# Optimization experiments

Hardware: AMD Instinct MI355X
Metric: run time of the kernel (lower is better)

Reference implementation:

```python
import jax, jax.numpy as jnp
import numpy as np

def setup_inputs() -> dict:
    key = jax.random.key(0)
    k1, k2 = jax.random.split(key)
    user_embeddings = jax.random.normal(k1, (1024, 64), dtype=jnp.float32)
    movie_embeddings = jax.random.normal(k2, (50000, 64), dtype=jnp.float32)
    return {"user_embeddings": user_embeddings, "movie_embeddings": movie_embeddings}

def reference(user_embeddings, movie_embeddings):
    # square_of_sum[b,m] = (sum_k u[b,k] m[m,k])^2
    square_of_sum = jnp.matmul(user_embeddings, movie_embeddings.T) ** 2
    # sum_of_square[b,m] = sum_k (u[b,k] m[m,k])^2 = (u^2) @ (m^2)^T
    # Algebraically identical to the original's broadcast (B, M, D) intermediate,
    # but computed as a second GEMM on squared embeddings.
    sum_of_square = jnp.matmul(user_embeddings ** 2, (movie_embeddings ** 2).T)
    interaction = 0.5 * (square_of_sum - sum_of_square)
    return interaction
```

## Files before the change

### kernel.cpp

```cpp
#include <hip/hip_runtime.h>

typedef short short8 __attribute__((ext_vector_type(8)));
typedef float f32x4 __attribute__((ext_vector_type(4)));

#define DK 64

__device__ __forceinline__ short f2bf(float x) {
    unsigned u = __builtin_bit_cast(unsigned, x);
    unsigned r = (u + 0x7fffu + ((u >> 16) & 1u)) >> 16;
    return (short)r;
}

__device__ __forceinline__ void gl_lds16(const void* g, void* l) {
    __builtin_amdgcn_global_load_lds(
        (const __attribute__((address_space(1))) unsigned int*)g,
        (__attribute__((address_space(3))) unsigned int*)l, 16, 0, 0);
}

__global__ __launch_bounds__(256)
void fm_convert(const float* __restrict__ U, const float* __restrict__ M,
                short* __restrict__ ws, int NU, int NM, int NUP, int NMP) {
    int id = blockIdx.x * blockDim.x + threadIdx.x;
    int total = (NUP + NMP) * 8;
    if (id >= total) return;
    int rowg = id >> 3;
    int p = id & 7;
    const float* src; short *dv, *dq; int row, nvalid;
    if (rowg < NUP) {
        row = rowg; src = U; dv = ws; dq = ws + (size_t)NUP * DK; nvalid = NU;
    } else {
        row = rowg - NUP; src = M;
        dv = ws + (size_t)2 * NUP * DK; dq = dv + (size_t)NMP * DK; nvalid = NM;
    }
    short8 v8 = {0,0,0,0,0,0,0,0}, q8 = {0,0,0,0,0,0,0,0};
    if (row < nvalid) {
        int cp = p ^ (row & 7);
        const float* s = src + (size_t)row * DK + cp * 8;
        float4 a = *(const float4*)(s);
        float4 b = *(const float4*)(s + 4);
        v8 = (short8){ f2bf(a.x), f2bf(a.y), f2bf(a.z), f2bf(a.w),
                       f2bf(b.x), f2bf(b.y), f2bf(b.z), f2bf(b.w) };
        q8 = (short8){ f2bf(a.x*a.x), f2bf(a.y*a.y), f2bf(a.z*a.z), f2bf(a.w*a.w),
                       f2bf(b.x*b.x), f2bf(b.y*b.y), f2bf(b.z*b.z), f2bf(b.w*b.w) };
    }
    *(short8*)(dv + (size_t)row * DK + p * 8) = v8;
    *(short8*)(dq + (size_t)row * DK + p * 8) = q8;
}

#define BM 64
#define BN 128

__global__ __launch_bounds__(256, 3)
void fm_gemm(const short* __restrict__ ws, float* __restrict__ out,
             int NM, int NMP, int NUP) {
    __shared__ short sA [BM * DK];
    __shared__ short sA2[BM * DK];
    __shared__ short sB [BN * DK];
    __shared__ short sB2[BN * DK];

    const int t = threadIdx.x;
    const int lane = t & 63;
    const int w = t >> 6;
    const int wr = w >> 1;
    const int wc = w & 1;
    const int lr = lane & 15;
    const int lk = lane >> 4;

    const int mbase = blockIdx.x * BM;
    const int nbase = blockIdx.y * BN;

    const short* gU  = ws;
    const short* gU2 = ws + (size_t)NUP * DK;
    const short* gM  = ws + (size_t)2 * NUP * DK;
    const short* gM2 = gM + (size_t)NMP * DK;

    {
        const short* srcA  = gU  + (size_t)mbase * DK;
        const short* srcA2 = gU2 + (size_t)mbase * DK;
        const short* srcB  = gM  + (size_t)nbase * DK;
        const short* srcB2 = gM2 + (size_t)nbase * DK;
        const int lo = lane * 8;
#pragma unroll
        for (int i = 0; i < 2; ++i) {
            const int ch = w * 2 + i;
            gl_lds16(srcA  + ch * 512 + lo, sA  + ch * 512);
            gl_lds16(srcA2 + ch * 512 + lo, sA2 + ch * 512);
        }
#pragma unroll
        for (int i = 0; i < 4; ++i) {
            const int ch = w * 4 + i;
            gl_lds16(srcB  + ch * 512 + lo, sB  + ch * 512);
            gl_lds16(srcB2 + ch * 512 + lo, sB2 + ch * 512);
        }
    }
    __syncthreads();

    f32x4 accS[2][4], accQ[2][4];
#pragma unroll
    for (int m = 0; m < 2; ++m)
#pragma unroll
        for (int n = 0; n < 4; ++n) {
            accS[m][n] = (f32x4){0.f, 0.f, 0.f, 0.f};
            accQ[m][n] = (f32x4){0.f, 0.f, 0.f, 0.f};
        }

#pragma unroll
    for (int ks = 0; ks < 2; ++ks) {
        const int c = ks * 4 + lk;
        short8 af[2], a2f[2], bf[4], b2f[4];
#pragma unroll
        for (int m = 0; m < 2; ++m) {
            const int row = wr * 32 + m * 16 + lr;
            const int idx = row * DK + ((c ^ (row & 7)) << 3);
            af[m]  = *(const short8*)&sA [idx];
            a2f[m] = *(const short8*)&sA2[idx];
        }
#pragma unroll
        for (int n = 0; n < 4; ++n) {
            const int row = wc * 64 + n * 16 + lr;
            const int idx = row * DK + ((c ^ (row & 7)) << 3);
            bf[n]  = *(const short8*)&sB [idx];
            b2f[n] = *(const short8*)&sB2[idx];
        }
#pragma unroll
        for (int m = 0; m < 2; ++m)
#pragma unroll
            for (int n = 0; n < 4; ++n) {
                accS[m][n] = __builtin_amdgcn_mfma_f32_16x16x32_bf16(af[m],  bf[n],  accS[m][n], 0, 0, 0);
                accQ[m][n] = __builtin_amdgcn_mfma_f32_16x16x32_bf16(a2f[m], b2f[n], accQ[m][n], 0, 0, 0);
            }
    }

#pragma unroll
    for (int m = 0; m < 2; ++m) {
        const int grow0 = mbase + wr * 32 + m * 16 + lk * 4;
#pragma unroll
        for (int n = 0; n < 4; ++n) {
            const int gcol = nbase + wc * 64 + n * 16 + lr;
            if (gcol < NM) {
                f32x4 s = accS[m][n];
                f32x4 q = accQ[m][n];
#pragma unroll
                for (int r = 0; r < 4; ++r)
                    out[(size_t)(grow0 + r) * NM + gcol] = 0.5f * (s[r] * s[r] - q[r]);
            }
        }
    }
}

__global__ __launch_bounds__(256, 2)
void fm_fallback(const float* __restrict__ U, const float* __restrict__ M,
                 float* __restrict__ out, int NU, int NM) {
    __shared__ short sA [128 * DK];
    __shared__ short sA2[128 * DK];
    __shared__ short sB [128 * DK];
    __shared__ short sB2[128 * DK];

    const int t = threadIdx.x;
    const int lane = t & 63;
    const int w = t >> 6;
    const int wr = w >> 1;
    const int wc = w & 1;
    const int lr = lane & 15;
    const int lk = lane >> 4;

    const int mbase = blockIdx.x * 128;
    const int nbase = blockIdx.y * 128;

    const int r0 = t >> 4;
    const int c4 = t & 15;
    const int chunk = c4 >> 1;
    const int sub = c4 & 1;

    typedef short short4v __attribute__((ext_vector_type(4)));
#pragma unroll
    for (int i = 0; i < 8; ++i) {
        const int r = r0 + i * 16;
        const int sidx = r * DK + ((chunk ^ (r & 7)) << 3) + (sub << 2);
        {
            float4 v = make_float4(0.f, 0.f, 0.f, 0.f);
            const int gr = mbase + r;
            if (gr < NU) v = *(const float4*)(U + (size_t)gr * DK + c4 * 4);
            short4v b  = { f2bf(v.x), f2bf(v.y), f2bf(v.z), f2bf(v.w) };
            short4v b2 = { f2bf(v.x*v.x), f2bf(v.y*v.y), f2bf(v.z*v.z), f2bf(v.w*v.w) };
            *(short4v*)&sA[sidx] = b; *(short4v*)&sA2[sidx] = b2;
        }
        {
            float4 v = make_float4(0.f, 0.f, 0.f, 0.f);
            const int gr = nbase + r;
            if (gr < NM) v = *(const float4*)(M + (size_t)gr * DK + c4 * 4);
            short4v b  = { f2bf(v.x), f2bf(v.y), f2bf(v.z), f2bf(v.w) };
            short4v b2 = { f2bf(v.x*v.x), f2bf(v.y*v.y), f2bf(v.z*v.z), f2bf(v.w*v.w) };
            *(short4v*)&sB[sidx] = b; *(short4v*)&sB2[sidx] = b2;
        }
    }
    __syncthreads();

    f32x4 accS[4][4], accQ[4][4];
#pragma unroll
    for (int m = 0; m < 4; ++m)
#pragma unroll
        for (int n = 0; n < 4; ++n) {
            accS[m][n] = (f32x4){0.f,0.f,0.f,0.f};
            accQ[m][n] = (f32x4){0.f,0.f,0.f,0.f};
        }
#pragma unroll
    for (int ks = 0; ks < 2; ++ks) {
        short8 af[4], a2f[4], bfr[4], b2f[4];
        const int c = ks * 4 + lk;
#pragma unroll
        for (int m = 0; m < 4; ++m) {
            const int row = wr * 64 + m * 16 + lr;
            const int idx = row * DK + ((c ^ (row & 7)) << 3);
            af[m] = *(const short8*)&sA[idx]; a2f[m] = *(const short8*)&sA2[idx];
        }
#pragma unroll
        for (int n = 0; n < 4; ++n) {
            const int row = wc * 64 + n * 16 + lr;
            const int idx = row * DK + ((c ^ (row & 7)) << 3);
            bfr[n] = *(const short8*)&sB[idx]; b2f[n] = *(const short8*)&sB2[idx];
        }
#pragma unroll
        for (int m = 0; m < 4; ++m)
#pragma unroll
            for (int n = 0; n < 4; ++n) {
                accS[m][n] = __builtin_amdgcn_mfma_f32_16x16x32_bf16(af[m],  bfr[n], accS[m][n], 0, 0, 0);
                accQ[m][n] = __builtin_amdgcn_mfma_f32_16x16x32_bf16(a2f[m], b2f[n], accQ[m][n], 0, 0, 0);
            }
    }
#pragma unroll
    for (int m = 0; m < 4; ++m) {
        const int grow0 = mbase + wr * 64 + m * 16 + lk * 4;
#pragma unroll
        for (int n = 0; n < 4; ++n) {
            const int gcol = nbase + wc * 64 + n * 16 + lr;
            if (gcol < NM) {
                f32x4 s = accS[m][n]; f32x4 q = accQ[m][n];
#pragma unroll
                for (int r = 0; r < 4; ++r) {
                    const int grow = grow0 + r;
                    if (grow < NU)
                        out[(size_t)grow * NM + gcol] = 0.5f * (s[r]*s[r] - q[r]);
                }
            }
        }
    }
}

extern "C" void kernel_launch(void* const* d_in, const int* in_sizes, int n_in,
                              void* d_out, int out_size, void* d_ws, size_t ws_size,
                              hipStream_t stream) {
    const float* U = (const float*)d_in[0];
    const float* M = (const float*)d_in[1];
    float* out = (float*)d_out;
    const int NU = in_sizes[0] / DK;
    const int NM = in_sizes[1] / DK;
    const int NUP = ((NU + 63) / 64) * 64;
    const int NMP = ((NM + 127) / 128) * 128;
    const size_t need = (size_t)(NUP + NMP) * DK * 2 * sizeof(short);

    if ((NU % 64 == 0) && ws_size >= need) {
        short* ws = (short*)d_ws;
        const int tasks = (NUP + NMP) * 8;
        fm_convert<<<(tasks + 255) / 256, 256, 0, stream>>>(U, M, ws, NU, NM, NUP, NMP);
        dim3 grid(NU / BM, NMP / BN);
        fm_gemm<<<grid, dim3(256), 0, stream>>>(ws, out, NM, NMP, NUP);
    } else {
        dim3 grid((NU + 127) / 128, (NM + 127) / 128);
        fm_fallback<<<grid, dim3(256), 0, stream>>>(U, M, out, NU, NM);
    }
}
```

Before: 59.96 us.

## Drop LDS staging, keep movie fragments in registers and loop over user tiles

The GEMM kernel no longer stages tiles in shared memory. Each wave loads its 32 movie rows' bf16 fragments straight into registers once and reuses them across four 64-row user tiles, loading user fragments directly from global memory, which the L2 cache should serve because the user matrix is small. Operands are swapped so each lane holds four consecutive output columns, which allows 16-byte nontemporal stores to cut write traffic on the roughly 200 MB output. The cost is more global or L2 loads for the user data, lower occupancy (launch bounds 2), and a stricter fast-path condition requiring NU divisible by 256 and NM divisible by 4.

```diff
diff --git a/kernel.cpp b/kernel.cpp
--- a/kernel.cpp
+++ b/kernel.cpp
@@ -4,17 +4,12 @@
 typedef float f32x4 __attribute__((ext_vector_type(4)));
 
 #define DK 64
+#define TUSR 4
 
 __device__ __forceinline__ short f2bf(float x) {
     unsigned u = __builtin_bit_cast(unsigned, x);
     unsigned r = (u + 0x7fffu + ((u >> 16) & 1u)) >> 16;
     return (short)r;
-}
-
-__device__ __forceinline__ void gl_lds16(const void* g, void* l) {
-    __builtin_amdgcn_global_load_lds(
-        (const __attribute__((address_space(1))) unsigned int*)g,
-        (__attribute__((address_space(3))) unsigned int*)l, 16, 0, 0);
 }
 
 __global__ __launch_bounds__(256)
@@ -34,8 +29,7 @@
     }
     short8 v8 = {0,0,0,0,0,0,0,0}, q8 = {0,0,0,0,0,0,0,0};
     if (row < nvalid) {
-        int cp = p ^ (row & 7);
-        const float* s = src + (size_t)row * DK + cp * 8;
+        const float* s = src + (size_t)row * DK + p * 8;
         float4 a = *(const float4*)(s);
         float4 b = *(const float4*)(s + 4);
         v8 = (short8){ f2bf(a.x), f2bf(a.y), f2bf(a.z), f2bf(a.w),
@@ -47,102 +41,79 @@
     *(short8*)(dq + (size_t)row * DK + p * 8) = q8;
 }
 
-#define BM 64
-#define BN 128
-
-__global__ __launch_bounds__(256, 3)
+__global__ __launch_bounds__(256, 2)
 void fm_gemm(const short* __restrict__ ws, float* __restrict__ out,
              int NM, int NMP, int NUP) {
-    __shared__ short sA [BM * DK];
-    __shared__ short sA2[BM * DK];
-    __shared__ short sB [BN * DK];
-    __shared__ short sB2[BN * DK];
-
     const int t = threadIdx.x;
     const int lane = t & 63;
     const int w = t >> 6;
-    const int wr = w >> 1;
-    const int wc = w & 1;
     const int lr = lane & 15;
     const int lk = lane >> 4;
 
-    const int mbase = blockIdx.x * BM;
-    const int nbase = blockIdx.y * BN;
+    const int nb = blockIdx.y * 128 + w * 32;
 
     const short* gU  = ws;
     const short* gU2 = ws + (size_t)NUP * DK;
     const short* gM  = ws + (size_t)2 * NUP * DK;
     const short* gM2 = gM + (size_t)NMP * DK;
 
-    {
-        const short* srcA  = gU  + (size_t)mbase * DK;
-        const short* srcA2 = gU2 + (size_t)mbase * DK;
-        const short* srcB  = gM  + (size_t)nbase * DK;
-        const short* srcB2 = gM2 + (size_t)nbase * DK;
-        const int lo = lane * 8;
-#pragma unroll
-        for (int i = 0; i < 2; ++i) {
-            const int ch = w * 2 + i;
-            gl_lds16(srcA  + ch * 512 + lo, sA  + ch * 512);
-            gl_lds16(srcA2 + ch * 512 + lo, sA2 + ch * 512);
-        }
-#pragma unroll
-        for (int i = 0; i < 4; ++i) {
-            const int ch = w * 4 + i;
-            gl_lds16(srcB  + ch * 512 + lo, sB  + ch * 512);
-            gl_lds16(srcB2 + ch * 512 + lo, sB2 + ch * 512);
-        }
-    }
-    __syncthreads();
-
-    f32x4 accS[2][4], accQ[2][4];
-#pragma unroll
-    for (int m = 0; m < 2; ++m)
-#pragma unroll
-        for (int n = 0; n < 4; ++n) {
-            accS[m][n] = (f32x4){0.f, 0.f, 0.f, 0.f};
-            accQ[m][n] = (f32x4){0.f, 0.f, 0.f, 0.f};
-        }
-
-#pragma unroll
-    for (int ks = 0; ks < 2; ++ks) {
-        const int c = ks * 4 + lk;
-        short8 af[2], a2f[2], bf[4], b2f[4];
-#pragma unroll
-        for (int m = 0; m < 2; ++m) {
-            const int row = wr * 32 + m * 16 + lr;
-            const int idx = row * DK + ((c ^ (row & 7)) << 3);
-            af[m]  = *(const short8*)&sA [idx];
-            a2f[m] = *(const short8*)&sA2[idx];
-        }
-#pragma unroll
-        for (int n = 0; n < 4; ++n) {
-            const int row = wc * 64 + n * 16 + lr;
-            const int idx = row * DK + ((c ^ (row & 7)) << 3);
-            bf[n]  = *(const short8*)&sB [idx];
-            b2f[n] = *(const short8*)&sB2[idx];
-        }
-#pragma unroll
-        for (int m = 0; m < 2; ++m)
-#pragma unroll
-            for (int n = 0; n < 4; ++n) {
-                accS[m][n] = __builtin_amdgcn_mfma_f32_16x16x32_bf16(af[m],  bf[n],  accS[m][n], 0, 0, 0);
-                accQ[m][n] = __builtin_amdgcn_mfma_f32_16x16x32_bf16(a2f[m], b2f[n], accQ[m][n], 0, 0, 0);
-            }
-    }
-
-#pragma unroll
-    for (int m = 0; m < 2; ++m) {
-        const int grow0 = mbase + wr * 32 + m * 16 + lk * 4;
-#pragma unroll
-        for (int n = 0; n < 4; ++n) {
-            const int gcol = nbase + wc * 64 + n * 16 + lr;
-            if (gcol < NM) {
-                f32x4 s = accS[m][n];
-                f32x4 q = accQ[m][n];
-#pragma unroll
-                for (int r = 0; r < 4; ++r)
-                    out[(size_t)(grow0 + r) * NM + gcol] = 0.5f * (s[r] * s[r] - q[r]);
+    short8 bv[2][2], bq[2][2];
+#pragma unroll
+    for (int n = 0; n < 2; ++n)
+#pragma unroll
+        for (int ks = 0; ks < 2; ++ks) {
+            const size_t a = (size_t)(nb + n * 16 + lr) * DK + (ks * 4 + lk) * 8;
+            bv[n][ks] = *(const short8*)(gM  + a);
+            bq[n][ks] = *(const short8*)(gM2 + a);
+        }
+
+    const int ub0 = blockIdx.x * (64 * TUSR);
+#pragma unroll
+    for (int tt = 0; tt < TUSR; ++tt) {
+        const int ub = ub0 + tt * 64;
+        short8 av[4][2], aq[4][2];
+#pragma unroll
+        for (int m = 0; m < 4; ++m)
+#pragma unroll
+            for (int ks = 0; ks < 2; ++ks) {
+                const size_t a = (size_t)(ub + m * 16 + lr) * DK + (ks * 4 + lk) * 8;
+                av[m][ks] = *(const short8*)(gU  + a);
+                aq[m][ks] = *(const short8*)(gU2 + a);
+            }
+
+        f32x4 s[4][2], q[4][2];
+#pragma unroll
+        for (int m = 0; m < 4; ++m)
+#pragma unroll
+            for (int n = 0; n < 2; ++n) {
+                s[m][n] = (f32x4){0.f, 0.f, 0.f, 0.f};
+                q[m][n] = (f32x4){0.f, 0.f, 0.f, 0.f};
+            }
+
+#pragma unroll
+        for (int m = 0; m < 4; ++m)
+#pragma unroll
+            for (int n = 0; n < 2; ++n)
+#pragma unroll
+                for (int ks = 0; ks < 2; ++ks) {
+                    s[m][n] = __builtin_amdgcn_mfma_f32_16x16x32_bf16(bv[n][ks], av[m][ks], s[m][n], 0, 0, 0);
+                    q[m][n] = __builtin_amdgcn_mfma_f32_16x16x32_bf16(bq[n][ks], aq[m][ks], q[m][n], 0, 0, 0);
+                }
+
+#pragma unroll
+        for (int m = 0; m < 4; ++m) {
+            float* rowp = out + (size_t)(ub + m * 16 + lr) * NM;
+#pragma unroll
+            for (int n = 0; n < 2; ++n) {
+                const int col = nb + n * 16 + lk * 4;
+                if (col < NM) {
+                    f32x4 sv = s[m][n], qv = q[m][n];
+                    f32x4 r;
+#pragma unroll
+                    for (int i = 0; i < 4; ++i)
+                        r[i] = 0.5f * (sv[i] * sv[i] - qv[i]);
+                    __builtin_nontemporal_store(r, (f32x4*)(rowp + col));
+                }
             }
         }
     }
@@ -255,15 +226,15 @@
     float* out = (float*)d_out;
     const int NU = in_sizes[0] / DK;
     const int NM = in_sizes[1] / DK;
-    const int NUP = ((NU + 63) / 64) * 64;
+    const int NUP = NU;
     const int NMP = ((NM + 127) / 128) * 128;
     const size_t need = (size_t)(NUP + NMP) * DK * 2 * sizeof(short);
 
-    if ((NU % 64 == 0) && ws_size >= need) {
+    if ((NU % (64 * TUSR) == 0) && (NM % 4 == 0) && ws_size >= need) {
         short* ws = (short*)d_ws;
         const int tasks = (NUP + NMP) * 8;
         fm_convert<<<(tasks + 255) / 256, 256, 0, stream>>>(U, M, ws, NU, NM, NUP, NMP);
-        dim3 grid(NU / BM, NMP / BN);
+        dim3 grid(NU / (64 * TUSR), NMP / 128);
         fm_gemm<<<grid, dim3(256), 0, stream>>>(ws, out, NM, NMP, NUP);
     } else {
         dim3 grid((NU + 127) / 128, (NM + 127) / 128);
```

After: 87.54 us. 1.46x slower.
